# Kernel tuning notes

Measured on AMD Instinct MI355X. Metric: run time of the kernel, lower is better.

Reference implementation:

```python
import jax, jax.numpy as jnp
import numpy as np

W_PRIOR_STD = 1.0          # w_prior_stddev
OBS_STD = 1.0              # observational_noise_stddev
EPS = 1e-7                 # keras backend.epsilon()
B, E, K, C = 64, 32, 128, 512


def setup_inputs() -> dict:
    key = jax.random.key(0)
    k1, k2, k3, k4 = jax.random.split(key, 4)
    x = jax.random.normal(k1, (B, E, C), jnp.float32)
    prior_memory_mean = jax.random.normal(k2, (K, C), jnp.float32)  # truncated_normal(0,1) init
    prior_log_variance_scale = jax.random.uniform(k3, (), jnp.float32)  # scalar weight (init zeros; nonzero for testing)
    log_w_stddev = jnp.float32(0.3)  # constant(initial_w_stddev) init
    z_noise = jax.random.normal(k4, (E, B, C), jnp.float32)  # reparam noise for z_distribution.sample()
    return {"x": x, "prior_memory_mean": prior_memory_mean,
            "prior_log_variance_scale": prior_log_variance_scale,
            "log_w_stddev": log_w_stddev, "z_noise": z_noise}


def _kl_w(w, sw, k):
    # KL( N(w, sw^2 I_k) || N(0, w_prior^2 I_k) ), w_prior = 1
    return 0.5 * (k * sw * sw + jnp.sum(w * w, axis=-1) - k - 2.0 * k * jnp.log(sw))


def reference(x, prior_memory_mean, prior_log_variance_scale, log_w_stddev, z_noise):
    b, e, c = x.shape
    k = prior_memory_mean.shape[0]
    dt = x.dtype
    sw = jnp.exp(log_w_stddev)                      # w_stddev
    lam = (OBS_STD ** 2) / (W_PRIOR_STD ** 2)       # l2 regularizer in w-solve
    I_k = jnp.eye(k, dtype=dt)

    # prior state (tiled over batch)
    M0 = jnp.broadcast_to(prior_memory_mean[None], (b, k, c)) + jnp.zeros((b, k, c), dt)
    var = prior_log_variance_scale + EPS
    U0 = jnp.broadcast_to(var * I_k, (b, k, k)) + jnp.zeros((b, k, k), dt)

    z = jnp.transpose(x, (1, 0, 2))  # [E,B,C]

    def solve_w(M, z_t):
        # least squares: w = (M M^T + lam I)^{-1} M z  -> [B,K]
        A = jnp.einsum('bkc,blc->bkl', M, M) + lam * I_k
        rhs = jnp.einsum('bkc,bc->bk', M, z_t)
        return jnp.linalg.solve(A, rhs[..., None])[..., 0]

    def step(carry, z_t):
        M, U = carry                                    # [B,K,C], [B,K,K]
        w = solve_w(M, z_t)                             # memory sample == mean; iteration_count == 1
        delta = z_t - jnp.einsum('bk,bkc->bc', w, M)    # prediction delta [B,C]
        wU = jnp.einsum('bk,bkl->bl', w, U)             # cross variance [B,K]
        sigma = jnp.sum(wU * w, axis=-1) + OBS_STD ** 2 # z episode covariance [B]
        gain = wU / sigma[:, None]                      # [B,K]
        M_new = M + gain[..., None] * delta[:, None, :] # rank-1 Kalman update
        U_new = U - jnp.einsum('bk,bl->bkl', gain, wU)
        return (M_new, U_new), _kl_w(w, sw, k)          # per-step w divergence [B]

    (M_post, U_post), kl_episode = jax.lax.scan(step, (M0, U0), z)  # kl_episode [E,B]

    # read memory: batched solve with shared Gram matrix over episode
    A = jnp.einsum('bkc,blc->bkl', M_post, M_post) + lam * I_k
    rhs = jnp.einsum('bkc,ebc->bke', M_post, z)
    w_read = jnp.transpose(jnp.linalg.solve(A, rhs), (2, 0, 1))     # [E,B,K]
    z_mean = jnp.einsum('ebk,bkc->ebc', w_read, M_post)
    kl_read = _kl_w(w_read, sw, k)                                  # [E,B]

    total_divergence = jnp.mean(kl_episode + kl_read)               # add_loss value
    z_sample = z_mean + OBS_STD * z_noise                           # reparameterized sample
    return jnp.transpose(z_sample, (1, 0, 2)), total_divergence
```

## Files before the change

kernel.cpp:

```cpp
#include <hip/hip_runtime.h>

#define BB 64
#define EE 32
#define KK 128
#define CC 512
#define V0EPS 1e-7f

#define LTR 132
#define PTS 132
#define LKM 36
#define L36 36
#define LWT 176
#define SEG(i) ((((i) >> 4) * 20) + ((i) & 15))

#define SC_S2  0
#define SC_SIG 1
#define SC_KL  2
#define SC_B1  3
#define SC_B2  4
#define SC_R11 5
#define SC_R12 6
#define SC_R22 7

__device__ __forceinline__ float wsum64(float v) {
#pragma unroll
  for (int m = 32; m >= 1; m >>= 1) v += __shfl_xor(v, m, 64);
  return v;
}

__device__ __forceinline__ float wsum32(float v) {
#pragma unroll
  for (int m = 16; m >= 1; m >>= 1) v += __shfl_xor(v, m, 64);
  return v;
}

__device__ __forceinline__ float dot4(const float4 a, const float4 b) {
  return a.x * b.x + a.y * b.y + a.z * b.z + a.w * b.w;
}

__global__ __launch_bounds__(256) void a0_kernel(const float* __restrict__ M0,
                                                 float* __restrict__ wsA0) {
  __shared__ __align__(16) float sRow[CC];
  const int k = blockIdx.x >> 2, quarter = blockIdx.x & 3;
  for (int c = threadIdx.x; c < CC; c += 256) sRow[c] = M0[k * CC + c];
  __syncthreads();
  const int wv = threadIdx.x >> 6, ln = threadIdx.x & 63;
  const float4* zr = (const float4*)(sRow + 8 * ln);
  const float4 z0 = zr[0], z1 = zr[1];
  for (int li = 0; li < 8; ++li) {
    const int l = quarter * 32 + wv * 8 + li;
    const float4* rp = (const float4*)(M0 + l * CC + 8 * ln);
    const float4 a = rp[0], b = rp[1];
    float s = dot4(a, z0) + dot4(b, z1);
    s = wsum64(s);
    if (ln == 0) wsA0[k * KK + l] = s + (l == k ? 1.0f : 0.0f);
  }
}

__global__ __launch_bounds__(1024) void psinv_kernel(const float* __restrict__ x,
                                                     const float* __restrict__ M0,
                                                     float* __restrict__ wsP,
                                                     float* __restrict__ wsSp,
                                                     const float* __restrict__ A0g,
                                                     float* __restrict__ Ainv0) {
  __shared__ __align__(16) float zAll[32][520];
  __shared__ __align__(16) float Mch[2][16][520];
  __shared__ __align__(16) float sFb[2][2][128];
  __shared__ __align__(16) float sPv[2][2][256];
  const int tid = threadIdx.x;

  if (blockIdx.x > 0) {
    const int b = (blockIdx.x - 1) >> 2, kq = (blockIdx.x - 1) & 3;
    {
      const float4* x4 = (const float4*)(x + (size_t)b * EE * CC);
#pragma unroll
      for (int i = 0; i < 4; i++) {
        const int F = tid + 1024 * i, e = F >> 7, c4 = F & 127;
        ((float4*)zAll[e])[c4] = x4[F];
      }
    }
    const float4* M4 = (const float4*)M0;
    const int srow = tid >> 7, sc4 = tid & 127;
    const int kbase = kq * 32;
    float4 st0 = M4[(kbase + srow) * 128 + sc4];
    float4 st1 = M4[(kbase + 8 + srow) * 128 + sc4];
    int buf = 0;
    const int p = tid & 7;
    const int ep = (tid >> 3) & 15;
    const int kp = tid >> 7;
#pragma unroll 1
    for (int kc = 0; kc < 2; ++kc) {
      ((float4*)Mch[buf][srow])[sc4] = st0;
      ((float4*)Mch[buf][8 + srow])[sc4] = st1;
      __syncthreads();
      if (kc == 0) {
        st0 = M4[(kbase + 16 + srow) * 128 + sc4];
        st1 = M4[(kbase + 24 + srow) * 128 + sc4];
      }
      float s00 = 0, s01 = 0, s10 = 0, s11 = 0;
      const float* m0 = Mch[buf][kp];
      const float* m1 = Mch[buf][kp + 8];
      const float* z0 = zAll[2 * ep];
      const float* z1 = zAll[2 * ep + 1];
#pragma unroll
      for (int u = 0; u < 16; u++) {
        const int c = 4 * p + 32 * u;
        const float4 a0 = *(const float4*)(m0 + c);
        const float4 a1 = *(const float4*)(m1 + c);
        const float4 b0 = *(const float4*)(z0 + c);
        const float4 b1 = *(const float4*)(z1 + c);
        s00 += dot4(a0, b0); s01 += dot4(a0, b1);
        s10 += dot4(a1, b0); s11 += dot4(a1, b1);
      }
#pragma unroll
      for (int m = 1; m <= 4; m <<= 1) {
        s00 += __shfl_xor(s00, m, 64); s01 += __shfl_xor(s01, m, 64);
        s10 += __shfl_xor(s10, m, 64); s11 += __shfl_xor(s11, m, 64);
      }
      if (p == 0) {
        float* Pb = wsP + (size_t)b * KK * EE;
        Pb[(kbase + kc * 16 + kp) * EE + 2 * ep] = s00;
        Pb[(kbase + kc * 16 + kp) * EE + 2 * ep + 1] = s01;
        Pb[(kbase + kc * 16 + kp + 8) * EE + 2 * ep] = s10;
        Pb[(kbase + kc * 16 + kp + 8) * EE + 2 * ep + 1] = s11;
      }
      buf ^= 1;
    }
    {
      const int e = tid >> 5, f = tid & 31;
      const float4* ze = ((const float4*)zAll[e]) + 32 * kq;
      const float4* zf = ((const float4*)zAll[f]) + 32 * kq;
      float a0 = 0, a1 = 0, a2 = 0, a3 = 0;
#pragma unroll 4
      for (int u = 0; u < 32; u++) {
        const float4 A = ze[u], Bq = zf[u];
        a0 += A.x * Bq.x; a1 += A.y * Bq.y; a2 += A.z * Bq.z; a3 += A.w * Bq.w;
      }
      wsSp[((size_t)b * 4 + kq) * 1024 + e * EE + f] = (a0 + a1) + (a2 + a3);
    }
  } else {
    const int r = tid >> 3, q = tid & 7;
    float wreg[16], vreg[16];
    {
      const float4* a4 = (const float4*)(A0g + r * KK + 16 * q);
#pragma unroll
      for (int u = 0; u < 4; u++) {
        const float4 t4 = a4[u];
        wreg[4 * u] = t4.x; wreg[4 * u + 1] = t4.y; wreg[4 * u + 2] = t4.z; wreg[4 * u + 3] = t4.w;
      }
#pragma unroll
      for (int c = 0; c < 16; c++) vreg[c] = (16 * q + c == r) ? 1.0f : 0.0f;
    }
    if (q == 0) { sFb[0][0][r] = wreg[0]; sFb[0][1][r] = wreg[1]; }
    if (r == 0) {
#pragma unroll
      for (int c = 0; c < 16; c++) { sPv[0][0][16 * q + c] = wreg[c]; sPv[0][0][128 + 16 * q + c] = vreg[c]; }
    }
    if (r == 1) {
#pragma unroll
      for (int c = 0; c < 16; c++) { sPv[0][1][16 * q + c] = wreg[c]; sPv[0][1][128 + 16 * q + c] = vreg[c]; }
    }
    __syncthreads();
#pragma unroll 1
    for (int jj = 0; jj < 64; ++jj) {
      const int j = 2 * jj, db = jj & 1, dn = db ^ 1;
      const float* c0 = sFb[db][0];
      const float* c1 = sFb[db][1];
      const float* rj = sPv[db][0];
      const float* rj1 = sPv[db][1];
      const float p00 = c0[j], p10 = c0[j + 1], p01 = c1[j], p11 = c1[j + 1];
      const float rp00 = 1.0f / p00;
      const float g = p10 * rp00;
      const float rp11 = 1.0f / (p11 - g * p01);
      const float alpha = (r == j) ? 0.0f : c0[r] * rp00;
      const float beta = (r == j + 1) ? 0.0f : (c1[r] - alpha * p01) * rp11;
      const float ca = alpha - beta * g, cb = beta;
      if (16 * q + 15 >= j) {
        const float4* w0 = (const float4*)(rj + 16 * q);
        const float4* w1 = (const float4*)(rj1 + 16 * q);
#pragma unroll
        for (int u = 0; u < 4; u++) {
          const float4 a0 = w0[u], a1 = w1[u];
          wreg[4 * u]     -= ca * a0.x + cb * a1.x;
          wreg[4 * u + 1] -= ca * a0.y + cb * a1.y;
          wreg[4 * u + 2] -= ca * a0.z + cb * a1.z;
          wreg[4 * u + 3] -= ca * a0.w + cb * a1.w;
        }
      }
      if (16 * q <= j + 1) {
        const float4* v0 = (const float4*)(rj + 128 + 16 * q);
        const float4* v1 = (const float4*)(rj1 + 128 + 16 * q);
#pragma unroll
        for (int u = 0; u < 4; u++) {
          const float4 a0 = v0[u], a1 = v1[u];
          vreg[4 * u]     -= ca * a0.x + cb * a1.x;
          vreg[4 * u + 1] -= ca * a0.y + cb * a1.y;
          vreg[4 * u + 2] -= ca * a0.z + cb * a1.z;
          vreg[4 * u + 3] -= ca * a0.w + cb * a1.w;
        }
      }
      if (jj + 1 < 64) {
        const int j2 = j + 2, j3 = j + 3;
        float w2 = 0.0f, w3 = 0.0f;
#pragma unroll
        for (int c = 0; c < 16; c++) {
          if (c == (j2 & 15)) w2 = wreg[c];
          if (c == (j3 & 15)) w3 = wreg[c];
        }
        if (q == (j2 >> 4)) sFb[dn][0][r] = w2;
        if (q == (j3 >> 4)) sFb[dn][1][r] = w3;
        if (r == j2) {
#pragma unroll
          for (int c = 0; c < 16; c++) { sPv[dn][0][16 * q + c] = wreg[c]; sPv[dn][0][128 + 16 * q + c] = vreg[c]; }
        }
        if (r == j3) {
#pragma unroll
          for (int c = 0; c < 16; c++) { sPv[dn][1][16 * q + c] = wreg[c]; sPv[dn][1][128 + 16 * q + c] = vreg[c]; }
        }
      }
      __syncthreads();
    }
    {
      float dval = 0.0f;
#pragma unroll
      for (int c = 0; c < 16; c++) if (c == (r & 15)) dval = wreg[c];
      if (q == (r >> 4)) sFb[0][0][r] = dval;
    }
    __syncthreads();
    {
      const float sc = 1.0f / sFb[0][0][r];
      float4* o4 = (float4*)(Ainv0 + r * KK + 16 * q);
#pragma unroll
      for (int u = 0; u < 4; u++) {
        float4 o;
        o.x = vreg[4 * u] * sc; o.y = vreg[4 * u + 1] * sc;
        o.z = vreg[4 * u + 2] * sc; o.w = vreg[4 * u + 3] * sc;
        o4[u] = o;
      }
    }
  }
}

__global__ __launch_bounds__(512) void scan_kernel(
    const float* __restrict__ Pg, const float* __restrict__ Sg,
    const float* __restrict__ scaleP, const float* __restrict__ Ainv0,
    float* __restrict__ wsKL, float* __restrict__ wsKLr, float* __restrict__ wsWt) {
  __shared__ __align__(16) float sPT[EE * PTS];
  __shared__ __align__(16) float sGT[EE * LTR];
  __shared__ __align__(16) float sEggT[EE * LTR];
  __shared__ __align__(16) float uni2[EE * LTR];
  __shared__ __align__(16) float uni3[KK * LKM];
  __shared__ __align__(16) float uni1[KK * LKM];
  __shared__ __align__(16) float sEk[KK * LKM];
  __shared__ __align__(16) float sS[EE * L36];
  __shared__ __align__(16) float sD[EE * L36];
  __shared__ __align__(16) float sW[160];
  __shared__ __align__(16) float sWU[160];
  __shared__ __align__(16) float sPu[160];
  __shared__ __align__(16) float sPm[160];
  __shared__ __align__(16) float sQ[160];
  __shared__ __align__(16) float sDz[EE];
  __shared__ __align__(16) float sDgw[EE];
  __shared__ __align__(16) float sQt[EE];
  __shared__ __align__(16) float sScal[16];

  float* sYT = uni2;
  float* sGk = uni3;
  float* sYk = uni1;

  const int tid = threadIdx.x, wv = tid >> 6, ln = tid & 63;
  const int mr = tid >> 2, mq = tid & 3;
  const int b = blockIdx.x;

  float areg[32];
  {
    const float4* a4 = (const float4*)(Ainv0 + mr * KK + 32 * mq);
#pragma unroll
    for (int u = 0; u < 8; u++) {
      const float4 t4 = a4[u];
      areg[4 * u] = t4.x; areg[4 * u + 1] = t4.y; areg[4 * u + 2] = t4.z; areg[4 * u + 3] = t4.w;
    }
  }
  {
    const float* Pb = Pg + (size_t)b * KK * EE;
#pragma unroll
    for (int i = 0; i < 8; i++) {
      const int idx = tid + 512 * i;
      sPT[(idx & 31) * PTS + (idx >> 5)] = Pb[idx];
    }
    const float* Sb = Sg + (size_t)b * 4096;
#pragma unroll
    for (int i = 0; i < 2; i++) {
      const int idx = tid + 512 * i;
      sS[(idx >> 5) * L36 + (idx & 31)] =
          Sb[idx] + Sb[idx + 1024] + Sb[idx + 2048] + Sb[idx + 3072];
    }
  }
  if (tid < 16) sScal[tid] = 0.0f;
  const float v0 = scaleP[0] + V0EPS;
  __syncthreads();
  {
    const float* xb = sPT + 32 * mq;
    float s = 0;
#pragma unroll
    for (int c = 0; c < 32; c++) s += areg[c] * xb[c];
    s += __shfl_xor(s, 1, 64); s += __shfl_xor(s, 2, 64);
    if (mq == 0) sW[SEG(mr)] = s;
  }
  __syncthreads();

#pragma unroll 1
  for (int t = 0; t < EE; ++t) {
    const bool hn = (t + 1 < EE);
    {
      const float* xb = sW + 40 * mq;
      float s = 0;
#pragma unroll
      for (int c = 0; c < 16; c++) s += areg[c] * xb[c];
#pragma unroll
      for (int c = 0; c < 16; c++) s += areg[16 + c] * xb[20 + c];
      s += __shfl_xor(s, 1, 64); s += __shfl_xor(s, 2, 64);
      if (mq == 0) sPm[SEG(mr)] = s;
    }
    if (tid < 256) {
      const int s8 = tid >> 3, p3 = tid & 7;
      if (s8 < t) {
        const float* gr = sGT + s8 * LTR + 16 * p3;
        const float* wr_ = sW + 20 * p3;
        float s = 0;
#pragma unroll
        for (int kk = 0; kk < 16; kk++) s += gr[kk] * wr_[kk];
        s += __shfl_xor(s, 1, 64); s += __shfl_xor(s, 2, 64); s += __shfl_xor(s, 4, 64);
        if (p3 == 0) sDgw[s8] = s;
      } else if (s8 == 31) {
        const float* wp = sW + 20 * p3;
        float s = 0;
#pragma unroll
        for (int kk = 0; kk < 16; kk++) s += wp[kk] * wp[kk];
        s += __shfl_xor(s, 1, 64); s += __shfl_xor(s, 2, 64); s += __shfl_xor(s, 4, 64);
        if (p3 == 0) sScal[SC_S2] = s;
      }
    } else {
      const int j = (tid - 256) >> 3, p3 = tid & 7;
      if (j < t) {
        const float* yr = sYT + j * LTR + 16 * p3;
        const float* wr_ = sW + 20 * p3;
        float s = 0;
#pragma unroll
        for (int kk = 0; kk < 16; kk++) s += yr[kk] * wr_[kk];
        s += __shfl_xor(s, 1, 64); s += __shfl_xor(s, 2, 64); s += __shfl_xor(s, 4, 64);
        if (p3 == 0) sQt[j] = s;
      }
    }
    __syncthreads();
    if (tid < 256) {
      const int k = tid >> 1, h = tid & 1;
      const float* yk = sYk + k * LKM + 16 * h;
      const float* qb = sQt + 16 * h;
      float a = 0;
#pragma unroll
      for (int u = 0; u < 16; u++) {
        const int j = 16 * h + u;
        a += (j < t) ? yk[u] * qb[u] : 0.0f;
      }
      a += __shfl_xor(a, 1, 64);
      if (h == 0) sWU[SEG(k)] = v0 * sW[SEG(k)] - a;
    } else if (tid < 384) {
      const int k = tid - 256;
      float a = sW[SEG(k)];
      const float* ek = sEk + k * LKM;
      const int nc = (t + 3) >> 2;
#pragma unroll 1
      for (int c4 = 0; c4 < nc; ++c4) {
        const float4 ev = *(const float4*)(ek + 4 * c4);
        const float4 dv = *(const float4*)(sDgw + 4 * c4);
        const int u0 = 4 * c4;
        a -= ((u0 + 0 < t) ? ev.x * dv.x : 0.0f) + ((u0 + 1 < t) ? ev.y * dv.y : 0.0f) +
             ((u0 + 2 < t) ? ev.z * dv.z : 0.0f) + ((u0 + 3 < t) ? ev.w * dv.w : 0.0f);
      }
      sEk[k * LKM + t] = a;
      sEggT[t * LTR + k] = a;
    } else if (tid < 448) {
      if (ln < 32) {
        const int r2 = ln;
        float a = (r2 == t) ? 1.0f : 0.0f;
        for (int s2 = 0; s2 < t; ++s2) a -= sDgw[s2] * sD[s2 * L36 + r2];
        sD[t * L36 + r2] = a;
      } else {
        const int k0 = (ln - 32) * 4;
        const float4 wv4 = *(const float4*)(sW + SEG(k0));
        const float4 pm4 = *(const float4*)(sPm + SEG(k0));
        float a = dot4(wv4, pm4);
        a = wsum32(a);
        if (ln == 32) sScal[SC_R22] = a;
      }
    } else {
      const float s2v = sScal[SC_S2];
      float a = (ln < t) ? sQt[ln] * sQt[ln] : 0.0f;
      a = wsum64(a);
      if (ln == 0) {
        sScal[SC_SIG] = v0 * s2v - a + 1.0f;
        sScal[SC_KL] += s2v;
      }
    }
    __syncthreads();
    {
      const float* xb = sWU + 40 * mq;
      float s = 0;
#pragma unroll
      for (int c = 0; c < 16; c++) s += areg[c] * xb[c];
#pragma unroll
      for (int c = 0; c < 16; c++) s += areg[16 + c] * xb[20 + c];
      s += __shfl_xor(s, 1, 64); s += __shfl_xor(s, 2, 64);
      if (mq == 0) sPu[SEG(mr)] = s;
    }
    if (tid < 256) {
      const int s4 = tid >> 3, p3 = tid & 7;
      if (hn && s4 <= t) {
        const float* er = sEggT + s4 * LTR + 16 * p3;
        const float* pr = sPT + (t + 1) * PTS + 16 * p3;
        float a = 0;
#pragma unroll
        for (int kk = 0; kk < 16; kk++) a -= er[kk] * pr[kk];
        const float4 dv = *(const float4*)(sD + s4 * L36 + 4 * p3);
        const float4 sv = *(const float4*)(sS + (t + 1) * L36 + 4 * p3);
        a += dot4(dv, sv);
        a += __shfl_xor(a, 1, 64); a += __shfl_xor(a, 2, 64); a += __shfl_xor(a, 4, 64);
        if (p3 == 0) sDz[s4] = a;
      }
    } else if (tid < 320) {
      float a = sEggT[t * LTR + ln] * sPT[t * PTS + ln] +
                sEggT[t * LTR + ln + 64] * sPT[t * PTS + ln + 64];
      a = wsum64(a);
      if (ln == 0) sScal[SC_B2] = a;
    } else if (tid < 384) {
      if (ln < 32) {
        float a = sD[t * L36 + ln] * sS[t * L36 + ln];
        a = wsum32(a);
        if (ln == 0) sScal[SC_B1] = a;
      } else {
        const int k0 = (ln - 32) * 4;
        const float4 wu4 = *(const float4*)(sWU + SEG(k0));
        const float4 pm4 = *(const float4*)(sPm + SEG(k0));
        float a = dot4(wu4, pm4);
        a = wsum32(a);
        if (ln == 32) sScal[SC_R12] = a;
      }
    } else if (tid < 448) {
      const float sig = sScal[SC_SIG];
      const float rsq = rsqrtf(sig);
#pragma unroll
      for (int u = 0; u < 2; u++) {
        const int k = ln + 64 * u;
        const float wu = sWU[SEG(k)];
        const float gv = wu / sig;
        const float yv = wu * rsq;
        sGT[t * LTR + k] = gv;
        sGk[k * LKM + t] = gv;
        sYT[t * LTR + k] = yv;
        sYk[k * LKM + t] = yv;
      }
    }
    __syncthreads();
    if (hn) {
      const float* gk = sGk + mr * LKM + 8 * mq;
      const float* dzb = sDz + 8 * mq;
      float a = 0;
#pragma unroll
      for (int u = 0; u < 8; u++) {
        const int s2 = 8 * mq + u;
        a += (s2 < t) ? gk[u] * dzb[u] : 0.0f;
      }
      a += __shfl_xor(a, 1, 64); a += __shfl_xor(a, 2, 64);
      if (mq == 0)
        sQ[SEG(mr)] = sPT[(t + 1) * PTS + mr] + a + (sWU[SEG(mr)] / sScal[SC_SIG]) * sDz[t];
    }
    if (wv == 0) {
      float a = sWU[SEG(ln)] * sPu[SEG(ln)] + sWU[SEG(ln + 64)] * sPu[SEG(ln + 64)];
      a = wsum64(a);
      if (ln == 0) sScal[SC_R11] = a;
    }
    __syncthreads();
    {
      const float4 sc0 = *(const float4*)(sScal);
      const float4 sc1 = *(const float4*)(sScal + 4);
      const float rs = 1.0f / sc0.y;
      const float beta = sc0.w - sc1.x - sc0.x;
      const float e11 = sc1.y * rs * rs;
      const float e12 = sc1.z * rs + 1.0f;
      const float e22 = sc1.w - beta;
      const float rd = 1.0f / (e11 * e22 - e12 * e12);
      const float t11 = e22 * rd, t12 = -e12 * rd, t22 = e11 * rd;
      const float u1r = sPu[SEG(mr)] * rs, u2r = sPm[SEG(mr)];
      const float* pub = sPu + 40 * mq;
      const float* pmb = sPm + 40 * mq;
#pragma unroll
      for (int c = 0; c < 16; c++) {
        const float u1c = pub[c] * rs;
        const float u2c = pmb[c];
        areg[c] -= u1r * (t11 * u1c + t12 * u2c) + u2r * (t12 * u1c + t22 * u2c);
      }
#pragma unroll
      for (int c = 0; c < 16; c++) {
        const float u1c = pub[20 + c] * rs;
        const float u2c = pmb[20 + c];
        areg[16 + c] -= u1r * (t11 * u1c + t12 * u2c) + u2r * (t12 * u1c + t22 * u2c);
      }
    }
    if (hn) {
      const float* xb = sQ + 40 * mq;
      float s = 0;
#pragma unroll
      for (int c = 0; c < 16; c++) s += areg[c] * xb[c];
#pragma unroll
      for (int c = 0; c < 16; c++) s += areg[16 + c] * xb[20 + c];
      s += __shfl_xor(s, 1, 64); s += __shfl_xor(s, 2, 64);
      if (mq == 0) sW[SEG(mr)] = s;
    }
    __syncthreads();
  }

  float* sR1T  = uni2;
  float* sGamT = uni2 + 1152;
  float* sRhsT = uni1;
  float* sWrT  = uni3;
  if (tid == 0) wsKL[b] = sScal[SC_KL];

#pragma unroll
  for (int h = 0; h < 2; ++h) {
    const int lin = tid + 512 * h, s = lin >> 5, e = lin & 31;
    const float4* er = (const float4*)(sEggT + s * LTR);
    const float4* pr = (const float4*)(sPT + e * PTS);
    float a = 0;
#pragma unroll 8
    for (int u = 0; u < 32; ++u) a -= dot4(er[u], pr[u]);
    const float4* dr = (const float4*)(sD + s * L36);
    const float4* sr = (const float4*)(sS + e * L36);
#pragma unroll
    for (int u = 0; u < 8; ++u) a += dot4(dr[u], sr[u]);
    sR1T[e * 36 + s] = a;
  }
  __syncthreads();
  {
    const int k = tid & 127, e4 = tid >> 7;
    float4 g0, g1, g2, g3, g4, g5, g6, g7;
    {
      const float4* gk = (const float4*)(sGk + k * LKM);
      g0 = gk[0]; g1 = gk[1]; g2 = gk[2]; g3 = gk[3];
      g4 = gk[4]; g5 = gk[5]; g6 = gk[6]; g7 = gk[7];
    }
#pragma unroll
    for (int u = 0; u < 8; ++u) {
      const int e = e4 * 8 + u;
      const float4* r1 = (const float4*)(sR1T + e * 36);
      float a = sPT[e * PTS + k];
      a += dot4(g0, r1[0]) + dot4(g1, r1[1]) + dot4(g2, r1[2]) + dot4(g3, r1[3]);
      a += dot4(g4, r1[4]) + dot4(g5, r1[5]) + dot4(g6, r1[6]) + dot4(g7, r1[7]);
      sRhsT[e * PTS + k] = a;
    }
  }
  __syncthreads();
#pragma unroll 2
  for (int e = 0; e < EE; ++e) {
    const float* xb = sRhsT + e * PTS + 32 * mq;
    float s = 0;
#pragma unroll
    for (int c = 0; c < 32; c++) s += areg[c] * xb[c];
    s += __shfl_xor(s, 1, 64); s += __shfl_xor(s, 2, 64);
    if (mq == 0) sWrT[e * PTS + mr] = s;
  }
  __syncthreads();
#pragma unroll
  for (int h = 0; h < 2; ++h) {
    const int lin = tid + 512 * h, s = lin >> 5, e = lin & 31;
    const float4* gr = (const float4*)(sGT + s * LTR);
    const float4* wr = (const float4*)(sWrT + e * PTS);
    float a = 0;
#pragma unroll 8
    for (int u = 0; u < 32; ++u) a += dot4(gr[u], wr[u]);
    sGamT[e * 36 + s] = a;
  }
  __syncthreads();
  {
    const int k = tid & 127, e4 = tid >> 7;
    float4 E0, E1, E2, E3, E4, E5, E6, E7;
    {
      const float4* ek = (const float4*)(sEk + k * LKM);
      E0 = ek[0]; E1 = ek[1]; E2 = ek[2]; E3 = ek[3];
      E4 = ek[4]; E5 = ek[5]; E6 = ek[6]; E7 = ek[7];
    }
#pragma unroll
    for (int u = 0; u < 8; ++u) {
      const int e = e4 * 8 + u;
      const float4* gm = (const float4*)(sGamT + e * 36);
      float a = sWrT[e * PTS + k];
      a -= dot4(E0, gm[0]) + dot4(E1, gm[1]) + dot4(E2, gm[2]) + dot4(E3, gm[3]);
      a -= dot4(E4, gm[4]) + dot4(E5, gm[5]) + dot4(E6, gm[6]) + dot4(E7, gm[7]);
      wsWt[(size_t)b * 5120 + e * 160 + k] = a;
    }
  }
  {
    const int e = tid & 31, sp = tid >> 5;
    float4 gm[8];
    {
      const float4* g4 = (const float4*)(sGamT + e * 36);
#pragma unroll
      for (int u = 0; u < 8; ++u) gm[u] = g4[u];
    }
#pragma unroll
    for (int h = 0; h < 2; ++h) {
      const int sp2 = sp + 16 * h;
      float a = 0;
#pragma unroll
      for (int u = 0; u < 8; ++u) {
        const float4 g = gm[u];
        a += sD[(4 * u + 0) * L36 + sp2] * g.x + sD[(4 * u + 1) * L36 + sp2] * g.y +
             sD[(4 * u + 2) * L36 + sp2] * g.z + sD[(4 * u + 3) * L36 + sp2] * g.w;
      }
      wsWt[(size_t)b * 5120 + e * 160 + 128 + sp2] = a;
    }
  }
  {
    const int e = tid >> 4, p = tid & 15;
    const float4* wr = (const float4*)(sWrT + e * PTS + 8 * p);
    const float4 w0 = wr[0], w1 = wr[1];
    float a = dot4(w0, w0) + dot4(w1, w1);
    a += __shfl_xor(a, 1, 64); a += __shfl_xor(a, 2, 64);
    a += __shfl_xor(a, 4, 64); a += __shfl_xor(a, 8, 64);
    if (p == 0) wsKLr[b * EE + e] = a;
  }
}

__global__ __launch_bounds__(512) void postBF_kernel(
    const float* __restrict__ wsWt, const float* __restrict__ x,
    const float* __restrict__ M0, const float* __restrict__ znoise,
    const float* __restrict__ wsKL, const float* __restrict__ wsKLr,
    const float* __restrict__ lwsP, float* __restrict__ out) {
  __shared__ __align__(16) float sWtT[32 * LWT];
  __shared__ __align__(16) float Mch[2 * 16 * 132];
  const int tid = threadIdx.x;

  if (blockIdx.x == 256) {
    float* sPp = sWtT;
    float s = 0.0f;
    if (tid < 64) s += wsKL[tid];
    for (int i = tid; i < 2048; i += 512) s += wsKLr[i];
    sPp[tid] = s;
    __syncthreads();
    for (int off = 256; off > 0; off >>= 1) {
      if (tid < off) sPp[tid] += sPp[tid + off];
      __syncthreads();
    }
    if (tid == 0) {
      const float lws = lwsP[0];
      const float sw2 = expf(2.0f * lws);
      out[(size_t)BB * EE * CC] =
          0.5f * sPp[0] / (float)(EE * BB) + (float)KK * (sw2 - 1.0f - 2.0f * lws);
    }
    return;
  }

  const int b = blockIdx.x >> 2, cq = blockIdx.x & 3;
  {
    const int e = tid >> 4, j = tid & 15;
    const float* Wg = wsWt + (size_t)b * 5120 + e * 160;
#pragma unroll
    for (int u = 0; u < 10; ++u) sWtT[e * LWT + j + 16 * u] = Wg[j + 16 * u];
  }
  const int srow = tid >> 5, sc4 = tid & 31;
  const int e = tid & 31, cs = tid >> 5;
  const float* xb = x + (size_t)b * EE * CC;
  const int cbase = cq * 128;
  float4 st = *(const float4*)(M0 + srow * CC + cbase + 4 * sc4);
  float acc[8];
#pragma unroll
  for (int u = 0; u < 8; u++) acc[u] = 0.0f;
  int buf = 0;
#pragma unroll 1
  for (int ch2 = 0; ch2 < 10; ++ch2) {
    *(float4*)(Mch + buf * 2112 + srow * 132 + 4 * sc4) = st;
    __syncthreads();
    if (ch2 + 1 < 10) {
      const int row = (ch2 + 1) * 16 + srow;
      st = (row < 128) ? *(const float4*)(M0 + row * CC + cbase + 4 * sc4)
                       : *(const float4*)(xb + (row - 128) * CC + cbase + 4 * sc4);
    }
    const float4* wt4 = (const float4*)(sWtT + e * LWT + ch2 * 16);
    const float4 wa = wt4[0], wb = wt4[1], wc = wt4[2], wd = wt4[3];
    const float wv16[16] = {wa.x, wa.y, wa.z, wa.w, wb.x, wb.y, wb.z, wb.w,
                            wc.x, wc.y, wc.z, wc.w, wd.x, wd.y, wd.z, wd.w};
#pragma unroll
    for (int kk = 0; kk < 16; ++kk) {
      const float* mrp = Mch + buf * 2112 + kk * 132 + cs * 8;
      const float4 m0 = *(const float4*)(mrp);
      const float4 m1 = *(const float4*)(mrp + 4);
      const float wk = wv16[kk];
      acc[0] += wk * m0.x; acc[1] += wk * m0.y; acc[2] += wk * m0.z; acc[3] += wk * m0.w;
      acc[4] += wk * m1.x; acc[5] += wk * m1.y; acc[6] += wk * m1.z; acc[7] += wk * m1.w;
    }
    buf ^= 1;
  }
  {
    const size_t ob = ((size_t)b * EE + e) * CC + cbase + cs * 8;
    const size_t nb = ((size_t)e * BB + b) * CC + cbase + cs * 8;
#pragma unroll
    for (int u = 0; u < 2; u++) {
      const float4 nz = *(const float4*)(znoise + nb + 4 * u);
      float4 o;
      o.x = acc[4 * u] + nz.x;     o.y = acc[4 * u + 1] + nz.y;
      o.z = acc[4 * u + 2] + nz.z; o.w = acc[4 * u + 3] + nz.w;
      *(float4*)(out + ob + 4 * u) = o;
    }
  }
}

extern "C" void kernel_launch(void* const* d_in, const int* in_sizes, int n_in,
                              void* d_out, int out_size, void* d_ws, size_t ws_size,
                              hipStream_t stream) {
  (void)in_sizes; (void)n_in; (void)out_size; (void)ws_size;
  const float* x = (const float*)d_in[0];
  const float* M0 = (const float*)d_in[1];
  const float* scaleP = (const float*)d_in[2];
  const float* lwsP = (const float*)d_in[3];
  const float* znoise = (const float*)d_in[4];
  float* out = (float*)d_out;

  float* ws = (float*)d_ws;
  float* wsP = ws;
  float* wsSp = wsP + 262144;
  float* wsA0 = wsSp + 262144;
  float* wsAinv0 = wsA0 + 16384;
  float* wsKL = wsAinv0 + 16384;
  float* wsKLr = wsKL + 64;
  float* wsWt = wsKLr + 2048;

  a0_kernel<<<512, 256, 0, stream>>>(M0, wsA0);
  psinv_kernel<<<257, 1024, 0, stream>>>(x, M0, wsP, wsSp, wsA0, wsAinv0);
  scan_kernel<<<BB, 512, 0, stream>>>(wsP, wsSp, scaleP, wsAinv0,
                                      wsKL, wsKLr, wsWt);
  postBF_kernel<<<257, 512, 0, stream>>>(wsWt, x, M0, znoise, wsKL, wsKLr, lwsP, out);
}
```

Before: 268.5 us.

## Block Gauss-Jordan inversion by four pivots per step to halve barriers

The 128x128 matrix inverse in the block-0 path of psinv_kernel now eliminates four pivot columns per iteration instead of two. It does this with a small 4x4 LDL-style factorization of the pivot block, so the loop runs 32 times instead of 64 and needs half as many __syncthreads barriers. The cost is more shared-memory staging, more scalar arithmetic and more register pressure per iteration, plus slightly different rounding order. Since this block runs alongside other blocks, its latency only matters if it sits on the critical path.

```diff
diff --git a/kernel.cpp b/kernel.cpp
--- a/kernel.cpp
+++ b/kernel.cpp
@@ -65,8 +65,8 @@
                                                      float* __restrict__ Ainv0) {
   __shared__ __align__(16) float zAll[32][520];
   __shared__ __align__(16) float Mch[2][16][520];
-  __shared__ __align__(16) float sFb[2][2][128];
-  __shared__ __align__(16) float sPv[2][2][256];
+  __shared__ __align__(16) float sFb[2][4][128];
+  __shared__ __align__(16) float sPv[2][4][256];
   const int tid = threadIdx.x;
 
   if (blockIdx.x > 0) {
@@ -151,71 +151,98 @@
 #pragma unroll
       for (int c = 0; c < 16; c++) vreg[c] = (16 * q + c == r) ? 1.0f : 0.0f;
     }
-    if (q == 0) { sFb[0][0][r] = wreg[0]; sFb[0][1][r] = wreg[1]; }
-    if (r == 0) {
-#pragma unroll
-      for (int c = 0; c < 16; c++) { sPv[0][0][16 * q + c] = wreg[c]; sPv[0][0][128 + 16 * q + c] = vreg[c]; }
-    }
-    if (r == 1) {
-#pragma unroll
-      for (int c = 0; c < 16; c++) { sPv[0][1][16 * q + c] = wreg[c]; sPv[0][1][128 + 16 * q + c] = vreg[c]; }
+    if (q == 0) {
+      sFb[0][0][r] = wreg[0]; sFb[0][1][r] = wreg[1];
+      sFb[0][2][r] = wreg[2]; sFb[0][3][r] = wreg[3];
+    }
+    if (r < 4) {
+#pragma unroll
+      for (int c = 0; c < 16; c++) {
+        sPv[0][r][16 * q + c] = wreg[c];
+        sPv[0][r][128 + 16 * q + c] = vreg[c];
+      }
     }
     __syncthreads();
 #pragma unroll 1
-    for (int jj = 0; jj < 64; ++jj) {
-      const int j = 2 * jj, db = jj & 1, dn = db ^ 1;
+    for (int jj = 0; jj < 32; ++jj) {
+      const int j = 4 * jj, db = jj & 1, dn = db ^ 1;
       const float* c0 = sFb[db][0];
       const float* c1 = sFb[db][1];
-      const float* rj = sPv[db][0];
-      const float* rj1 = sPv[db][1];
-      const float p00 = c0[j], p10 = c0[j + 1], p01 = c1[j], p11 = c1[j + 1];
+      const float* c2 = sFb[db][2];
+      const float* c3 = sFb[db][3];
+      const float* r0 = sPv[db][0];
+      const float* r1 = sPv[db][1];
+      const float* r2 = sPv[db][2];
+      const float* r3 = sPv[db][3];
+      const float p00 = c0[j],     p01 = c1[j],     p02 = c2[j],     p03 = c3[j];
+      const float p10 = c0[j + 1], p11 = c1[j + 1], p12 = c2[j + 1], p13 = c3[j + 1];
+      const float p20 = c0[j + 2], p21 = c1[j + 2], p22 = c2[j + 2], p23 = c3[j + 2];
+      const float p30 = c0[j + 3], p31 = c1[j + 3], p32 = c2[j + 3], p33 = c3[j + 3];
       const float rp00 = 1.0f / p00;
-      const float g = p10 * rp00;
-      const float rp11 = 1.0f / (p11 - g * p01);
-      const float alpha = (r == j) ? 0.0f : c0[r] * rp00;
-      const float beta = (r == j + 1) ? 0.0f : (c1[r] - alpha * p01) * rp11;
-      const float ca = alpha - beta * g, cb = beta;
+      const float g10 = p10 * rp00;
+      const float q11 = p11 - g10 * p01, q12 = p12 - g10 * p02, q13 = p13 - g10 * p03;
+      const float rq11 = 1.0f / q11;
+      const float g20 = p20 * rp00;
+      const float g21 = (p21 - g20 * p01) * rq11;
+      const float q22 = p22 - g20 * p02 - g21 * q12;
+      const float q23 = p23 - g20 * p03 - g21 * q13;
+      const float rq22 = 1.0f / q22;
+      const float g30 = p30 * rp00;
+      const float g31 = (p31 - g30 * p01) * rq11;
+      const float g32 = (p32 - g30 * p02 - g31 * q12) * rq22;
+      const float q33 = p33 - g30 * p03 - g31 * q13 - g32 * q23;
+      const float rq33 = 1.0f / q33;
+      const float f0 = (r == j) ? 0.0f : c0[r] * rp00;
+      const float f1 = (r == j + 1) ? 0.0f : (c1[r] - f0 * p01) * rq11;
+      const float f2 = (r == j + 2) ? 0.0f : (c2[r] - f0 * p02 - f1 * q12) * rq22;
+      const float f3 = (r == j + 3) ? 0.0f : (c3[r] - f0 * p03 - f1 * q13 - f2 * q23) * rq33;
+      const float cc3 = f3;
+      const float cc2 = f2 - cc3 * g32;
+      const float cc1 = f1 - cc2 * g21 - cc3 * g31;
+      const float cc0 = f0 - cc1 * g10 - cc2 * g20 - cc3 * g30;
       if (16 * q + 15 >= j) {
-        const float4* w0 = (const float4*)(rj + 16 * q);
-        const float4* w1 = (const float4*)(rj1 + 16 * q);
+        const float4* w0 = (const float4*)(r0 + 16 * q);
+        const float4* w1 = (const float4*)(r1 + 16 * q);
+        const float4* w2 = (const float4*)(r2 + 16 * q);
+        const float4* w3 = (const float4*)(r3 + 16 * q);
 #pragma unroll
         for (int u = 0; u < 4; u++) {
-          const float4 a0 = w0[u], a1 = w1[u];
-          wreg[4 * u]     -= ca * a0.x + cb * a1.x;
-          wreg[4 * u + 1] -= ca * a0.y + cb * a1.y;
-          wreg[4 * u + 2] -= ca * a0.z + cb * a1.z;
-          wreg[4 * u + 3] -= ca * a0.w + cb * a1.w;
+          const float4 a0 = w0[u], a1 = w1[u], a2 = w2[u], a3 = w3[u];
+          wreg[4 * u]     -= cc0 * a0.x + cc1 * a1.x + cc2 * a2.x + cc3 * a3.x;
+          wreg[4 * u + 1] -= cc0 * a0.y + cc1 * a1.y + cc2 * a2.y + cc3 * a3.y;
+          wreg[4 * u + 2] -= cc0 * a0.z + cc1 * a1.z + cc2 * a2.z + cc3 * a3.z;
+          wreg[4 * u + 3] -= cc0 * a0.w + cc1 * a1.w + cc2 * a2.w + cc3 * a3.w;
         }
       }
-      if (16 * q <= j + 1) {
-        const float4* v0 = (const float4*)(rj + 128 + 16 * q);
-        const float4* v1 = (const float4*)(rj1 + 128 + 16 * q);
+      if (16 * q <= j + 3) {
+        const float4* v0 = (const float4*)(r0 + 128 + 16 * q);
+        const float4* v1 = (const float4*)(r1 + 128 + 16 * q);
+        const float4* v2 = (const float4*)(r2 + 128 + 16 * q);
+        const float4* v3 = (const float4*)(r3 + 128 + 16 * q);
 #pragma unroll
         for (int u = 0; u < 4; u++) {
-          const float4 a0 = v0[u], a1 = v1[u];
-          vreg[4 * u]     -= ca * a0.x + cb * a1.x;
-          vreg[4 * u + 1] -= ca * a0.y + cb * a1.y;
-          vreg[4 * u + 2] -= ca * a0.z + cb * a1.z;
-          vreg[4 * u + 3] -= ca * a0.w + cb * a1.w;
+          const float4 a0 = v0[u], a1 = v1[u], a2 = v2[u], a3 = v3[u];
+          vreg[4 * u]     -= cc0 * a0.x + cc1 * a1.x + cc2 * a2.x + cc3 * a3.x;
+          vreg[4 * u + 1] -= cc0 * a0.y + cc1 * a1.y + cc2 * a2.y + cc3 * a3.y;
+          vreg[4 * u + 2] -= cc0 * a0.z + cc1 * a1.z + cc2 * a2.z + cc3 * a3.z;
+          vreg[4 * u + 3] -= cc0 * a0.w + cc1 * a1.w + cc2 * a2.w + cc3 * a3.w;
         }
       }
-      if (jj + 1 < 64) {
-        const int j2 = j + 2, j3 = j + 3;
-        float w2 = 0.0f, w3 = 0.0f;
-#pragma unroll
-        for (int c = 0; c < 16; c++) {
-          if (c == (j2 & 15)) w2 = wreg[c];
-          if (c == (j3 & 15)) w3 = wreg[c];
-        }
-        if (q == (j2 >> 4)) sFb[dn][0][r] = w2;
-        if (q == (j3 >> 4)) sFb[dn][1][r] = w3;
-        if (r == j2) {
-#pragma unroll
-          for (int c = 0; c < 16; c++) { sPv[dn][0][16 * q + c] = wreg[c]; sPv[dn][0][128 + 16 * q + c] = vreg[c]; }
-        }
-        if (r == j3) {
-#pragma unroll
-          for (int c = 0; c < 16; c++) { sPv[dn][1][16 * q + c] = wreg[c]; sPv[dn][1][128 + 16 * q + c] = vreg[c]; }
+      if (jj + 1 < 32) {
+#pragma unroll
+        for (int i = 0; i < 4; ++i) {
+          const int j2 = j + 4 + i;
+          float wv_ = 0.0f;
+#pragma unroll
+          for (int c = 0; c < 16; c++) if (c == (j2 & 15)) wv_ = wreg[c];
+          if (q == (j2 >> 4)) sFb[dn][i][r] = wv_;
+          if (r == j2) {
+#pragma unroll
+            for (int c = 0; c < 16; c++) {
+              sPv[dn][i][16 * q + c] = wreg[c];
+              sPv[dn][i][128 + 16 * q + c] = vreg[c];
+            }
+          }
         }
       }
       __syncthreads();
```

Measured after the change: 261.6 us, median of 2. 1.03x faster.
